# Kernel tuning notes

Hardware: AMD Instinct MI355X
Metric: run time of the kernel (lower is better)

## Reference

```python
import jax, jax.numpy as jnp
import numpy as np

KERNEL_MUL = 2.0
KERNEL_NUM = 5


def _index_matrix(b: int) -> jnp.ndarray:
    # non-linear JMMD index matrix (linear=False)
    im = np.zeros((2 * b, 2 * b), dtype=np.float32)
    off = 1.0 / float(b * (b - 1))
    eye = np.eye(b, dtype=bool)
    im[:b, :b][~eye] = off
    im[b:, b:][~eye] = off
    im[:b, b:] = -1.0 / float(b * b)
    im[b:, :b] = -1.0 / float(b * b)
    return jnp.asarray(im)


def _gaussian_kernel(source, target):
    total = jnp.concatenate([source, target], axis=0)  # [2b, d]
    n = total.shape[0]
    sq = jnp.sum(total * total, axis=1)  # [2b]
    # pairwise squared L2 via Gram matrix (same math as expand/diff/sum)
    l2 = sq[:, None] + sq[None, :] - 2.0 * (total @ total.T)
    l2 = jnp.maximum(l2, 0.0)
    # bandwidth computed on detached distances (torch uses .data)
    bw = jax.lax.stop_gradient(jnp.sum(l2)) / float(n * n - n)
    bw = bw / (KERNEL_MUL ** (KERNEL_NUM // 2))
    k = jnp.zeros_like(l2)
    for i in range(KERNEL_NUM):
        k = k + jnp.exp(-l2 / (bw * (KERNEL_MUL ** i)))
    return k


def setup_inputs() -> dict:
    key = jax.random.key(0)
    k1, k2, k3, k4 = jax.random.split(key, 4)
    b, d1, d2 = 2048, 4096, 2048
    return {
        "z1_s": jax.random.normal(k1, (b, d1), dtype=jnp.float32),
        "z1_t": jax.random.normal(k2, (b, d1), dtype=jnp.float32),
        "z2_s": jax.random.normal(k3, (b, d2), dtype=jnp.float32),
        "z2_t": jax.random.normal(k4, (b, d2), dtype=jnp.float32),
    }


def reference(z1_s, z1_t, z2_s, z2_t):
    b = z1_s.shape[0]
    index_matrix = _index_matrix(b)  # [2b, 2b]
    kernel_matrix = _gaussian_kernel(z1_s, z1_t) * _gaussian_kernel(z2_s, z2_t)
    loss = jnp.sum(kernel_matrix * index_matrix) + 2.0 / float(b - 1)
    return loss
```

## Files before the change

### kernel.cpp

```cpp
#include <hip/hip_runtime.h>
#include <cstdint>

#define NTOT 4096
#define BHALF 2048
#define D1 4096
#define D2 2048
#define TT 32
#define NTILES 528

typedef __attribute__((ext_vector_type(4))) float f32x4;
typedef __attribute__((ext_vector_type(4))) int i32x4;
typedef __attribute__((ext_vector_type(8))) int i32x8;

__device__ __forceinline__ void glds16(const uint8_t* g, uint8_t* l) {
    __builtin_amdgcn_global_load_lds(
        (const __attribute__((address_space(1))) void*)(uintptr_t)g,
        (__attribute__((address_space(3))) void*)(uint32_t)(uintptr_t)l,
        16, 0, 0);
}

__device__ __forceinline__ i32x4 ldsr(uint32_t addr) {
    i32x4 r;
    asm volatile("ds_read_b128 %0, %1" : "=v"(r) : "v"(addr));
    return r;
}

__device__ __forceinline__ float fp8dec(unsigned b) {
    unsigned e = (b >> 3) & 15u, m = b & 7u;
    float v = e ? __uint_as_float(((e + 120u) << 23) | (m << 20))
                : (float)m * 0.001953125f;
    return (b & 128u) ? -v : v;
}

__global__ void prep_kernel(const float* __restrict__ z1s, const float* __restrict__ z1t,
                            const float* __restrict__ z2s, const float* __restrict__ z2t,
                            float* __restrict__ sq1, float* __restrict__ sq2,
                            uint8_t* __restrict__ t1f8, uint8_t* __restrict__ t2f8,
                            float* __restrict__ s1, float* __restrict__ s2) {
    int bid = blockIdx.x;
    int tid = threadIdx.x;
    if (bid == 0) { for (int i = tid; i < 4096; i += 256) s1[i] = 0.f; }
    if (bid == 1) { for (int i = tid; i < 2048; i += 256) s2[i] = 0.f; }
    int which = bid >> 12;
    int row = bid & 4095;
    int d = which ? D2 : D1;
    const float* s_ = which ? z2s : z1s;
    const float* t_ = which ? z2t : z1t;
    const float* src = (row < BHALF) ? s_ + (size_t)row * d : t_ + (size_t)(row - BHALF) * d;
    uint8_t* dst = (which ? t2f8 : t1f8) + (size_t)row * d;
    float* sq = which ? sq2 : sq1;
    const float4* src4 = (const float4*)src;
    float a = 0.f;
    int n8 = d >> 3;
    for (int i = tid; i < n8; i += 256) {
        float4 v0 = src4[2 * i], v1 = src4[2 * i + 1];
        a += v0.x * v0.x + v0.y * v0.y + v0.z * v0.z + v0.w * v0.w;
        a += v1.x * v1.x + v1.y * v1.y + v1.z * v1.z + v1.w * v1.w;
        int w0 = __builtin_amdgcn_cvt_pk_fp8_f32(v0.x, v0.y, 0, 0);
        w0 = __builtin_amdgcn_cvt_pk_fp8_f32(v0.z, v0.w, w0, 1);
        int w1 = __builtin_amdgcn_cvt_pk_fp8_f32(v1.x, v1.y, 0, 0);
        w1 = __builtin_amdgcn_cvt_pk_fp8_f32(v1.z, v1.w, w1, 1);
        ((uint2*)dst)[i] = uint2{(unsigned)w0, (unsigned)w1};
    }
    for (int o = 32; o; o >>= 1) a += __shfl_down(a, o);
    __shared__ float sh[4];
    int lane = tid & 63, w = tid >> 6;
    if (lane == 0) sh[w] = a;
    __syncthreads();
    if (tid == 0) sq[row] = sh[0] + sh[1] + sh[2] + sh[3];
}

__global__ void colsum_fp8_kernel(const uint8_t* __restrict__ t1f8,
                                  const uint8_t* __restrict__ t2f8,
                                  float* __restrict__ s1, float* __restrict__ s2) {
    int bid = blockIdx.x;
    int which = bid >= 256;
    int local = which ? bid - 256 : bid;
    int d = which ? D2 : D1;
    int colchunks = d >> 10;
    int cb = local % colchunks, rb = local / colchunks;
    const uint8_t* base = which ? t2f8 : t1f8;
    float* s = which ? s2 : s1;
    int col = (cb << 10) + threadIdx.x * 4;
    int r0 = rb * 64;
    float a0 = 0.f, a1 = 0.f, a2 = 0.f, a3 = 0.f;
    const uint8_t* p = base + (size_t)r0 * d + col;
#pragma unroll 4
    for (int r = 0; r < 64; ++r) {
        uchar4 u = *(const uchar4*)(p + (size_t)r * d);
        a0 += fp8dec(u.x); a1 += fp8dec(u.y); a2 += fp8dec(u.z); a3 += fp8dec(u.w);
    }
    atomicAdd(&s[col], a0); atomicAdd(&s[col + 1], a1);
    atomicAdd(&s[col + 2], a2); atomicAdd(&s[col + 3], a3);
}

__global__ void finalize_kernel(const float* __restrict__ s1, const float* __restrict__ s2,
                                const float* __restrict__ sq1, const float* __restrict__ sq2,
                                float* __restrict__ acc, float* __restrict__ out) {
    int tid = threadIdx.x;
    float a1 = 0.f, a2 = 0.f, q1 = 0.f, q2 = 0.f;
    for (int i = tid; i < 4096; i += 256) { float v = s1[i]; a1 += v * v; q1 += sq1[i]; q2 += sq2[i]; }
    for (int i = tid; i < 2048; i += 256) { float v = s2[i]; a2 += v * v; }
    for (int o = 32; o; o >>= 1) {
        a1 += __shfl_down(a1, o); a2 += __shfl_down(a2, o);
        q1 += __shfl_down(q1, o); q2 += __shfl_down(q2, o);
    }
    __shared__ float sh[4][4];
    int lane = tid & 63, w = tid >> 6;
    if (lane == 0) { sh[0][w] = a1; sh[1][w] = a2; sh[2][w] = q1; sh[3][w] = q2; }
    __syncthreads();
    if (tid == 0) {
        double ss1 = (double)sh[0][0] + sh[0][1] + sh[0][2] + sh[0][3];
        double ss2 = (double)sh[1][0] + sh[1][1] + sh[1][2] + sh[1][3];
        double t1 = (double)sh[2][0] + sh[2][1] + sh[2][2] + sh[2][3];
        double t2 = (double)sh[3][0] + sh[3][1] + sh[3][2] + sh[3][3];
        double S1 = 2.0 * (double)NTOT * t1 - 2.0 * ss1;
        double S2 = 2.0 * (double)NTOT * t2 - 2.0 * ss2;
        const double L2E = 1.4426950408889634;
        double nn = (double)NTOT * (double)(NTOT - 1);
        acc[2] = (float)(nn * L2E / (4.0 * S1));
        acc[3] = (float)(nn * L2E / (4.0 * S2));
        out[0] = 2.0f / (float)(BHALF - 1);
    }
}

__device__ __forceinline__ void gemm_mx_pipe(const uint8_t* __restrict__ ga,
                                             const uint8_t* __restrict__ gb,
                                             int d,
                                             uint8_t* A0, uint8_t* B0,
                                             uint8_t* A1, uint8_t* B1,
                                             f32x4 (&acc)[4][4], int wv, int lane,
                                             int wm, int wn, int lm, int quad) {
    int nsteps = d >> 7;
    int rsub = lane >> 3;
    int ql = (lane & 7) ^ rsub;
    const uint8_t* pa = ga + (size_t)(wv * 32 + rsub) * d + ql * 16;
    const uint8_t* pb = gb + (size_t)(wv * 32 + rsub) * d + ql * 16;
    uint8_t* dA[2] = { A0 + wv * 4096, A1 + wv * 4096 };
    uint8_t* dB[2] = { B0 + wv * 4096, B1 + wv * 4096 };
    uint32_t baseA[2] = { (uint32_t)(uintptr_t)A0, (uint32_t)(uintptr_t)A1 };
    uint32_t baseB[2] = { (uint32_t)(uintptr_t)B0, (uint32_t)(uintptr_t)B1 };
    int s0 = ((2 * quad) ^ (lm & 7)) * 16;
    int s1 = ((2 * quad + 1) ^ (lm & 7)) * 16;
    uint32_t offA[4], offB[4];
#pragma unroll
    for (int i = 0; i < 4; ++i) {
        offA[i] = (uint32_t)((wm * 64 + i * 16 + lm) * 128);
        offB[i] = (uint32_t)((wn * 64 + i * 16 + lm) * 128);
    }
#pragma unroll
    for (int i = 0; i < 4; ++i) {
        glds16(pa + (size_t)i * 8 * d, dA[0] + i * 1024);
        glds16(pb + (size_t)i * 8 * d, dB[0] + i * 1024);
    }
    for (int k = 0; k < nsteps; ++k) {
        int cur = k & 1, nxt = cur ^ 1;
        size_t koff = (size_t)((k + 1 < nsteps) ? (k + 1) : 0) << 7;
#pragma unroll
        for (int i = 0; i < 4; ++i) {
            glds16(pa + koff + (size_t)i * 8 * d, dA[nxt] + i * 1024);
            glds16(pb + koff + (size_t)i * 8 * d, dB[nxt] + i * 1024);
        }
        asm volatile("s_waitcnt vmcnt(8)\n\ts_barrier" ::: "memory");
        i32x4 a00, a01, a10, a11, a20, a21, a30, a31;
        i32x4 b00, b01, b10, b11, b20, b21, b30, b31;
        a00 = ldsr(baseA[cur] + offA[0] + s0); a01 = ldsr(baseA[cur] + offA[0] + s1);
        a10 = ldsr(baseA[cur] + offA[1] + s0); a11 = ldsr(baseA[cur] + offA[1] + s1);
        a20 = ldsr(baseA[cur] + offA[2] + s0); a21 = ldsr(baseA[cur] + offA[2] + s1);
        a30 = ldsr(baseA[cur] + offA[3] + s0); a31 = ldsr(baseA[cur] + offA[3] + s1);
        b00 = ldsr(baseB[cur] + offB[0] + s0); b01 = ldsr(baseB[cur] + offB[0] + s1);
        b10 = ldsr(baseB[cur] + offB[1] + s0); b11 = ldsr(baseB[cur] + offB[1] + s1);
        b20 = ldsr(baseB[cur] + offB[2] + s0); b21 = ldsr(baseB[cur] + offB[2] + s1);
        b30 = ldsr(baseB[cur] + offB[3] + s0); b31 = ldsr(baseB[cur] + offB[3] + s1);
        asm volatile("s_waitcnt lgkmcnt(0)"
                     : "+v"(a00), "+v"(a01), "+v"(a10), "+v"(a11),
                       "+v"(a20), "+v"(a21), "+v"(a30), "+v"(a31),
                       "+v"(b00), "+v"(b01), "+v"(b10), "+v"(b11),
                       "+v"(b20), "+v"(b21), "+v"(b30), "+v"(b31));
        union F { i32x4 h[2]; i32x8 v; };
        F ua[4], ub[4];
        ua[0].h[0] = a00; ua[0].h[1] = a01; ua[1].h[0] = a10; ua[1].h[1] = a11;
        ua[2].h[0] = a20; ua[2].h[1] = a21; ua[3].h[0] = a30; ua[3].h[1] = a31;
        ub[0].h[0] = b00; ub[0].h[1] = b01; ub[1].h[0] = b10; ub[1].h[1] = b11;
        ub[2].h[0] = b20; ub[2].h[1] = b21; ub[3].h[0] = b30; ub[3].h[1] = b31;
#pragma unroll
        for (int ni = 0; ni < 4; ++ni)
#pragma unroll
            for (int mi = 0; mi < 4; ++mi)
                acc[mi][ni] = __builtin_amdgcn_mfma_scale_f32_16x16x128_f8f6f4(
                    ua[mi].v, ub[ni].v, acc[mi][ni], 0, 0, 0, 0x7F7F7F7F, 0, 0x7F7F7F7F);
        asm volatile("s_barrier" ::: "memory");
    }
}

__global__ __launch_bounds__(256, 2) void jmmd_fused(
    const uint8_t* __restrict__ t1f8, const uint8_t* __restrict__ t2f8,
    const float* __restrict__ sq1, const float* __restrict__ sq2,
    const float* __restrict__ cv, float* __restrict__ out) {
    __shared__ alignas(16) uint8_t smem[4][16384];
    __shared__ float sqi1[128], sqj1[128], sqi2[128], sqj2[128];
    __shared__ float red[4];
    int tid = threadIdx.x;
    int ti = 0, r = blockIdx.x;
    while (r >= TT - ti) { r -= TT - ti; ++ti; }
    int tj = ti + r;
    int i0 = ti * 128, j0 = tj * 128;
    if (tid < 128) {
        sqi1[tid] = sq1[i0 + tid]; sqj1[tid] = sq1[j0 + tid];
        sqi2[tid] = sq2[i0 + tid]; sqj2[tid] = sq2[j0 + tid];
    }
    int lane = tid & 63, wv = tid >> 6;
    int wm = wv >> 1, wn = wv & 1, lm = lane & 15, quad = lane >> 4;
    f32x4 acc1[4][4] = {};
    f32x4 acc2[4][4] = {};
    gemm_mx_pipe(t1f8 + (size_t)i0 * D1, t1f8 + (size_t)j0 * D1, D1,
                 smem[0], smem[1], smem[2], smem[3], acc1, wv, lane, wm, wn, lm, quad);
    asm volatile("s_waitcnt vmcnt(0)\n\ts_barrier" ::: "memory");
    gemm_mx_pipe(t2f8 + (size_t)i0 * D2, t2f8 + (size_t)j0 * D2, D2,
                 smem[0], smem[1], smem[2], smem[3], acc2, wv, lane, wm, wn, lm, quad);
    float c1 = cv[0], c2 = cv[1];
    float local = 0.f;
    bool diag = (ti == tj);
#pragma unroll
    for (int mi = 0; mi < 4; ++mi) {
        int rbase = wm * 64 + mi * 16 + quad * 4;
#pragma unroll
        for (int ni = 0; ni < 4; ++ni) {
            int col = wn * 64 + ni * 16 + lm;
            float sb1 = sqj1[col], sb2 = sqj2[col];
#pragma unroll
            for (int rr = 0; rr < 4; ++rr) {
                int row = rbase + rr;
                float l2a = fmaxf(sqi1[row] + sb1 - 2.f * acc1[mi][ni][rr], 0.f);
                float l2b = fmaxf(sqi2[row] + sb2 - 2.f * acc2[mi][ni][rr], 0.f);
                float t1 = __builtin_amdgcn_exp2f(-l2a * c1);
                float k1 = t1; float u1 = t1 * t1; k1 += u1; u1 *= u1; k1 += u1; u1 *= u1; k1 += u1; u1 *= u1; k1 += u1;
                float t2 = __builtin_amdgcn_exp2f(-l2b * c2);
                float k2 = t2; float u2 = t2 * t2; k2 += u2; u2 *= u2; k2 += u2; u2 *= u2; k2 += u2; u2 *= u2; k2 += u2;
                float v = k1 * k2;
                if (diag && (row == col)) v = 0.f;
                local += v;
            }
        }
    }
    for (int o = 32; o; o >>= 1) local += __shfl_down(local, o);
    if (lane == 0) red[wv] = local;
    __syncthreads();
    if (tid == 0) {
        bool same = (i0 < BHALF) == (j0 < BHALF);
        float w = same ? (1.0f / ((float)BHALF * (float)(BHALF - 1)))
                       : (-1.0f / ((float)BHALF * (float)BHALF));
        if (!diag) w *= 2.f;
        atomicAdd(out, (red[0] + red[1] + red[2] + red[3]) * w);
    }
}

extern "C" void kernel_launch(void* const* d_in, const int* in_sizes, int n_in,
                              void* d_out, int out_size, void* d_ws, size_t ws_size,
                              hipStream_t stream) {
    const float* z1s = (const float*)d_in[0];
    const float* z1t = (const float*)d_in[1];
    const float* z2s = (const float*)d_in[2];
    const float* z2t = (const float*)d_in[3];
    float* out = (float*)d_out;

    float* ws = (float*)d_ws;
    float* sq1 = ws;
    float* sq2 = ws + 4096;
    float* s1  = ws + 8192;
    float* s2  = ws + 12288;
    float* acc = ws + 14336;
    uint8_t* t1f8 = (uint8_t*)(ws + 14344);
    uint8_t* t2f8 = t1f8 + (size_t)NTOT * D1;

    prep_kernel<<<8192, 256, 0, stream>>>(z1s, z1t, z2s, z2t, sq1, sq2, t1f8, t2f8, s1, s2);
    colsum_fp8_kernel<<<384, 256, 0, stream>>>(t1f8, t2f8, s1, s2);
    finalize_kernel<<<1, 256, 0, stream>>>(s1, s2, sq1, sq2, acc, out);
    jmmd_fused<<<NTILES, 256, 0, stream>>>(t1f8, t2f8, sq1, sq2, acc + 2, out);
}
```

Measured before the change: 277.3 us.

## Interleave LDS reads with MFMA in GEMM loop, merge prep rows, widen colsum loads

The GEMM inner loop now issues LDS reads in staged groups and waits on partial lgkmcnt counts. This lets the first MFMAs start while later fragments are still loading, and it raises wave priority around the MFMA groups. The prep kernel now handles both feature sets per row in one block, which halves the number of blocks. The column-sum kernel uses 16-byte loads with 16 accumulators per thread and fewer blocks. Fewer colsum blocks (96) may underfill the GPU, and more accumulator registers could raise register pressure.

```diff
diff --git a/kernel.cpp b/kernel.cpp
--- a/kernel.cpp
+++ b/kernel.cpp
@@ -37,61 +37,92 @@
                             float* __restrict__ sq1, float* __restrict__ sq2,
                             uint8_t* __restrict__ t1f8, uint8_t* __restrict__ t2f8,
                             float* __restrict__ s1, float* __restrict__ s2) {
-    int bid = blockIdx.x;
+    int row = blockIdx.x;
     int tid = threadIdx.x;
-    if (bid == 0) { for (int i = tid; i < 4096; i += 256) s1[i] = 0.f; }
-    if (bid == 1) { for (int i = tid; i < 2048; i += 256) s2[i] = 0.f; }
-    int which = bid >> 12;
-    int row = bid & 4095;
-    int d = which ? D2 : D1;
-    const float* s_ = which ? z2s : z1s;
-    const float* t_ = which ? z2t : z1t;
-    const float* src = (row < BHALF) ? s_ + (size_t)row * d : t_ + (size_t)(row - BHALF) * d;
-    uint8_t* dst = (which ? t2f8 : t1f8) + (size_t)row * d;
-    float* sq = which ? sq2 : sq1;
-    const float4* src4 = (const float4*)src;
-    float a = 0.f;
-    int n8 = d >> 3;
-    for (int i = tid; i < n8; i += 256) {
-        float4 v0 = src4[2 * i], v1 = src4[2 * i + 1];
-        a += v0.x * v0.x + v0.y * v0.y + v0.z * v0.z + v0.w * v0.w;
-        a += v1.x * v1.x + v1.y * v1.y + v1.z * v1.z + v1.w * v1.w;
-        int w0 = __builtin_amdgcn_cvt_pk_fp8_f32(v0.x, v0.y, 0, 0);
-        w0 = __builtin_amdgcn_cvt_pk_fp8_f32(v0.z, v0.w, w0, 1);
-        int w1 = __builtin_amdgcn_cvt_pk_fp8_f32(v1.x, v1.y, 0, 0);
-        w1 = __builtin_amdgcn_cvt_pk_fp8_f32(v1.z, v1.w, w1, 1);
-        ((uint2*)dst)[i] = uint2{(unsigned)w0, (unsigned)w1};
-    }
-    for (int o = 32; o; o >>= 1) a += __shfl_down(a, o);
-    __shared__ float sh[4];
+    if (row == 0) { for (int i = tid; i < 4096; i += 256) s1[i] = 0.f; }
+    if (row == 1) { for (int i = tid; i < 2048; i += 256) s2[i] = 0.f; }
+    bool lower = row < BHALF;
+    const float* src1 = lower ? z1s + (size_t)row * D1 : z1t + (size_t)(row - BHALF) * D1;
+    const float* src2 = lower ? z2s + (size_t)row * D2 : z2t + (size_t)(row - BHALF) * D2;
+    uint8_t* dst1 = t1f8 + (size_t)row * D1;
+    uint8_t* dst2 = t2f8 + (size_t)row * D2;
+    float a1 = 0.f, a2 = 0.f;
+    {
+        const float4* s4 = (const float4*)src1;
+        for (int i = tid; i < (D1 >> 3); i += 256) {
+            float4 v0 = s4[2 * i], v1 = s4[2 * i + 1];
+            a1 += v0.x * v0.x + v0.y * v0.y + v0.z * v0.z + v0.w * v0.w;
+            a1 += v1.x * v1.x + v1.y * v1.y + v1.z * v1.z + v1.w * v1.w;
+            int w0 = __builtin_amdgcn_cvt_pk_fp8_f32(v0.x, v0.y, 0, 0);
+            w0 = __builtin_amdgcn_cvt_pk_fp8_f32(v0.z, v0.w, w0, 1);
+            int w1 = __builtin_amdgcn_cvt_pk_fp8_f32(v1.x, v1.y, 0, 0);
+            w1 = __builtin_amdgcn_cvt_pk_fp8_f32(v1.z, v1.w, w1, 1);
+            ((uint2*)dst1)[i] = uint2{(unsigned)w0, (unsigned)w1};
+        }
+    }
+    {
+        const float4* s4 = (const float4*)src2;
+        for (int i = tid; i < (D2 >> 3); i += 256) {
+            float4 v0 = s4[2 * i], v1 = s4[2 * i + 1];
+            a2 += v0.x * v0.x + v0.y * v0.y + v0.z * v0.z + v0.w * v0.w;
+            a2 += v1.x * v1.x + v1.y * v1.y + v1.z * v1.z + v1.w * v1.w;
+            int w0 = __builtin_amdgcn_cvt_pk_fp8_f32(v0.x, v0.y, 0, 0);
+            w0 = __builtin_amdgcn_cvt_pk_fp8_f32(v0.z, v0.w, w0, 1);
+            int w1 = __builtin_amdgcn_cvt_pk_fp8_f32(v1.x, v1.y, 0, 0);
+            w1 = __builtin_amdgcn_cvt_pk_fp8_f32(v1.z, v1.w, w1, 1);
+            ((uint2*)dst2)[i] = uint2{(unsigned)w0, (unsigned)w1};
+        }
+    }
+    for (int o = 32; o; o >>= 1) {
+        a1 += __shfl_down(a1, o);
+        a2 += __shfl_down(a2, o);
+    }
+    __shared__ float sh[2][4];
     int lane = tid & 63, w = tid >> 6;
-    if (lane == 0) sh[w] = a;
+    if (lane == 0) { sh[0][w] = a1; sh[1][w] = a2; }
     __syncthreads();
-    if (tid == 0) sq[row] = sh[0] + sh[1] + sh[2] + sh[3];
+    if (tid == 0) {
+        sq1[row] = sh[0][0] + sh[0][1] + sh[0][2] + sh[0][3];
+        sq2[row] = sh[1][0] + sh[1][1] + sh[1][2] + sh[1][3];
+    }
 }
 
 __global__ void colsum_fp8_kernel(const uint8_t* __restrict__ t1f8,
                                   const uint8_t* __restrict__ t2f8,
                                   float* __restrict__ s1, float* __restrict__ s2) {
     int bid = blockIdx.x;
-    int which = bid >= 256;
-    int local = which ? bid - 256 : bid;
-    int d = which ? D2 : D1;
-    int colchunks = d >> 10;
-    int cb = local % colchunks, rb = local / colchunks;
-    const uint8_t* base = which ? t2f8 : t1f8;
-    float* s = which ? s2 : s1;
-    int col = (cb << 10) + threadIdx.x * 4;
-    int r0 = rb * 64;
-    float a0 = 0.f, a1 = 0.f, a2 = 0.f, a3 = 0.f;
+    int tid = threadIdx.x;
+    const uint8_t* base;
+    float* s;
+    int d, stripe, col;
+    if (bid < 64) {
+        base = t1f8; s = s1; d = D1;
+        stripe = bid; col = tid * 16;
+    } else {
+        base = t2f8; s = s2; d = D2;
+        int lb = bid - 64;
+        stripe = lb * 2 + (tid >> 7);
+        col = (tid & 127) * 16;
+    }
+    int r0 = stripe * 64;
     const uint8_t* p = base + (size_t)r0 * d + col;
+    float a[16];
+#pragma unroll
+    for (int i = 0; i < 16; ++i) a[i] = 0.f;
 #pragma unroll 4
     for (int r = 0; r < 64; ++r) {
-        uchar4 u = *(const uchar4*)(p + (size_t)r * d);
-        a0 += fp8dec(u.x); a1 += fp8dec(u.y); a2 += fp8dec(u.z); a3 += fp8dec(u.w);
-    }
-    atomicAdd(&s[col], a0); atomicAdd(&s[col + 1], a1);
-    atomicAdd(&s[col + 2], a2); atomicAdd(&s[col + 3], a3);
+        uint4 u = *(const uint4*)(p + (size_t)r * d);
+        unsigned w0 = u.x, w1 = u.y, w2 = u.z, w3 = u.w;
+#pragma unroll
+        for (int k = 0; k < 4; ++k) {
+            a[0 + k]  += fp8dec((w0 >> (8 * k)) & 255u);
+            a[4 + k]  += fp8dec((w1 >> (8 * k)) & 255u);
+            a[8 + k]  += fp8dec((w2 >> (8 * k)) & 255u);
+            a[12 + k] += fp8dec((w3 >> (8 * k)) & 255u);
+        }
+    }
+#pragma unroll
+    for (int i = 0; i < 16; ++i) atomicAdd(&s[col + i], a[i]);
 }
 
 __global__ void finalize_kernel(const float* __restrict__ s1, const float* __restrict__ s2,
@@ -162,34 +193,54 @@
             glds16(pb + koff + (size_t)i * 8 * d, dB[nxt] + i * 1024);
         }
         asm volatile("s_waitcnt vmcnt(8)\n\ts_barrier" ::: "memory");
-        i32x4 a00, a01, a10, a11, a20, a21, a30, a31;
-        i32x4 b00, b01, b10, b11, b20, b21, b30, b31;
-        a00 = ldsr(baseA[cur] + offA[0] + s0); a01 = ldsr(baseA[cur] + offA[0] + s1);
-        a10 = ldsr(baseA[cur] + offA[1] + s0); a11 = ldsr(baseA[cur] + offA[1] + s1);
-        a20 = ldsr(baseA[cur] + offA[2] + s0); a21 = ldsr(baseA[cur] + offA[2] + s1);
-        a30 = ldsr(baseA[cur] + offA[3] + s0); a31 = ldsr(baseA[cur] + offA[3] + s1);
-        b00 = ldsr(baseB[cur] + offB[0] + s0); b01 = ldsr(baseB[cur] + offB[0] + s1);
-        b10 = ldsr(baseB[cur] + offB[1] + s0); b11 = ldsr(baseB[cur] + offB[1] + s1);
-        b20 = ldsr(baseB[cur] + offB[2] + s0); b21 = ldsr(baseB[cur] + offB[2] + s1);
-        b30 = ldsr(baseB[cur] + offB[3] + s0); b31 = ldsr(baseB[cur] + offB[3] + s1);
+        i32x4 b00 = ldsr(baseB[cur] + offB[0] + s0), b01 = ldsr(baseB[cur] + offB[0] + s1);
+        i32x4 b10 = ldsr(baseB[cur] + offB[1] + s0), b11 = ldsr(baseB[cur] + offB[1] + s1);
+        i32x4 a00 = ldsr(baseA[cur] + offA[0] + s0), a01 = ldsr(baseA[cur] + offA[0] + s1);
+        i32x4 a10 = ldsr(baseA[cur] + offA[1] + s0), a11 = ldsr(baseA[cur] + offA[1] + s1);
+        i32x4 b20 = ldsr(baseB[cur] + offB[2] + s0), b21 = ldsr(baseB[cur] + offB[2] + s1);
+        i32x4 b30 = ldsr(baseB[cur] + offB[3] + s0), b31 = ldsr(baseB[cur] + offB[3] + s1);
+        i32x4 a20 = ldsr(baseA[cur] + offA[2] + s0), a21 = ldsr(baseA[cur] + offA[2] + s1);
+        i32x4 a30 = ldsr(baseA[cur] + offA[3] + s0), a31 = ldsr(baseA[cur] + offA[3] + s1);
+        union F { i32x4 h[2]; i32x8 v; };
+        F ua0, ua1, ua2, ua3, ub0, ub1, ub2, ub3;
+        asm volatile("s_waitcnt lgkmcnt(8)"
+                     : "+v"(b00), "+v"(b01), "+v"(b10), "+v"(b11),
+                       "+v"(a00), "+v"(a01), "+v"(a10), "+v"(a11));
+        __builtin_amdgcn_sched_barrier(0);
+        ub0.h[0] = b00; ub0.h[1] = b01; ub1.h[0] = b10; ub1.h[1] = b11;
+        ua0.h[0] = a00; ua0.h[1] = a01; ua1.h[0] = a10; ua1.h[1] = a11;
+        __builtin_amdgcn_s_setprio(1);
+        acc[0][0] = __builtin_amdgcn_mfma_scale_f32_16x16x128_f8f6f4(ua0.v, ub0.v, acc[0][0], 0, 0, 0, 0x7F7F7F7F, 0, 0x7F7F7F7F);
+        acc[0][1] = __builtin_amdgcn_mfma_scale_f32_16x16x128_f8f6f4(ua0.v, ub1.v, acc[0][1], 0, 0, 0, 0x7F7F7F7F, 0, 0x7F7F7F7F);
+        acc[1][0] = __builtin_amdgcn_mfma_scale_f32_16x16x128_f8f6f4(ua1.v, ub0.v, acc[1][0], 0, 0, 0, 0x7F7F7F7F, 0, 0x7F7F7F7F);
+        acc[1][1] = __builtin_amdgcn_mfma_scale_f32_16x16x128_f8f6f4(ua1.v, ub1.v, acc[1][1], 0, 0, 0, 0x7F7F7F7F, 0, 0x7F7F7F7F);
+        __builtin_amdgcn_s_setprio(0);
+        asm volatile("s_waitcnt lgkmcnt(4)"
+                     : "+v"(b20), "+v"(b21), "+v"(b30), "+v"(b31));
+        __builtin_amdgcn_sched_barrier(0);
+        ub2.h[0] = b20; ub2.h[1] = b21; ub3.h[0] = b30; ub3.h[1] = b31;
+        __builtin_amdgcn_s_setprio(1);
+        acc[0][2] = __builtin_amdgcn_mfma_scale_f32_16x16x128_f8f6f4(ua0.v, ub2.v, acc[0][2], 0, 0, 0, 0x7F7F7F7F, 0, 0x7F7F7F7F);
+        acc[0][3] = __builtin_amdgcn_mfma_scale_f32_16x16x128_f8f6f4(ua0.v, ub3.v, acc[0][3], 0, 0, 0, 0x7F7F7F7F, 0, 0x7F7F7F7F);
+        acc[1][2] = __builtin_amdgcn_mfma_scale_f32_16x16x128_f8f6f4(ua1.v, ub2.v, acc[1][2], 0, 0, 0, 0x7F7F7F7F, 0, 0x7F7F7F7F);
+        acc[1][3] = __builtin_amdgcn_mfma_scale_f32_16x16x128_f8f6f4(ua1.v, ub3.v, acc[1][3], 0, 0, 0, 0x7F7F7F7F, 0, 0x7F7F7F7F);
+        __builtin_amdgcn_s_setprio(0);
         asm volatile("s_waitcnt lgkmcnt(0)"
-                     : "+v"(a00), "+v"(a01), "+v"(a10), "+v"(a11),
-                       "+v"(a20), "+v"(a21), "+v"(a30), "+v"(a31),
-                       "+v"(b00), "+v"(b01), "+v"(b10), "+v"(b11),
-                       "+v"(b20), "+v"(b21), "+v"(b30), "+v"(b31));
-        union F { i32x4 h[2]; i32x8 v; };
-        F ua[4], ub[4];
-        ua[0].h[0] = a00; ua[0].h[1] = a01; ua[1].h[0] = a10; ua[1].h[1] = a11;
-        ua[2].h[0] = a20; ua[2].h[1] = a21; ua[3].h[0] = a30; ua[3].h[1] = a31;
-        ub[0].h[0] = b00; ub[0].h[1] = b01; ub[1].h[0] = b10; ub[1].h[1] = b11;
-        ub[2].h[0] = b20; ub[2].h[1] = b21; ub[3].h[0] = b30; ub[3].h[1] = b31;
-#pragma unroll
-        for (int ni = 0; ni < 4; ++ni)
-#pragma unroll
-            for (int mi = 0; mi < 4; ++mi)
-                acc[mi][ni] = __builtin_amdgcn_mfma_scale_f32_16x16x128_f8f6f4(
-                    ua[mi].v, ub[ni].v, acc[mi][ni], 0, 0, 0, 0x7F7F7F7F, 0, 0x7F7F7F7F);
+                     : "+v"(a20), "+v"(a21), "+v"(a30), "+v"(a31));
+        __builtin_amdgcn_sched_barrier(0);
         asm volatile("s_barrier" ::: "memory");
+        __builtin_amdgcn_sched_barrier(0);
+        ua2.h[0] = a20; ua2.h[1] = a21; ua3.h[0] = a30; ua3.h[1] = a31;
+        __builtin_amdgcn_s_setprio(1);
+        acc[2][0] = __builtin_amdgcn_mfma_scale_f32_16x16x128_f8f6f4(ua2.v, ub0.v, acc[2][0], 0, 0, 0, 0x7F7F7F7F, 0, 0x7F7F7F7F);
+        acc[2][1] = __builtin_amdgcn_mfma_scale_f32_16x16x128_f8f6f4(ua2.v, ub1.v, acc[2][1], 0, 0, 0, 0x7F7F7F7F, 0, 0x7F7F7F7F);
+        acc[2][2] = __builtin_amdgcn_mfma_scale_f32_16x16x128_f8f6f4(ua2.v, ub2.v, acc[2][2], 0, 0, 0, 0x7F7F7F7F, 0, 0x7F7F7F7F);
+        acc[2][3] = __builtin_amdgcn_mfma_scale_f32_16x16x128_f8f6f4(ua2.v, ub3.v, acc[2][3], 0, 0, 0, 0x7F7F7F7F, 0, 0x7F7F7F7F);
+        acc[3][0] = __builtin_amdgcn_mfma_scale_f32_16x16x128_f8f6f4(ua3.v, ub0.v, acc[3][0], 0, 0, 0, 0x7F7F7F7F, 0, 0x7F7F7F7F);
+        acc[3][1] = __builtin_amdgcn_mfma_scale_f32_16x16x128_f8f6f4(ua3.v, ub1.v, acc[3][1], 0, 0, 0, 0x7F7F7F7F, 0, 0x7F7F7F7F);
+        acc[3][2] = __builtin_amdgcn_mfma_scale_f32_16x16x128_f8f6f4(ua3.v, ub2.v, acc[3][2], 0, 0, 0, 0x7F7F7F7F, 0, 0x7F7F7F7F);
+        acc[3][3] = __builtin_amdgcn_mfma_scale_f32_16x16x128_f8f6f4(ua3.v, ub3.v, acc[3][3], 0, 0, 0, 0x7F7F7F7F, 0, 0x7F7F7F7F);
+        __builtin_amdgcn_s_setprio(0);
     }
 }
 
@@ -273,8 +324,8 @@
     uint8_t* t1f8 = (uint8_t*)(ws + 14344);
     uint8_t* t2f8 = t1f8 + (size_t)NTOT * D1;
 
-    prep_kernel<<<8192, 256, 0, stream>>>(z1s, z1t, z2s, z2t, sq1, sq2, t1f8, t2f8, s1, s2);
-    colsum_fp8_kernel<<<384, 256, 0, stream>>>(t1f8, t2f8, s1, s2);
+    prep_kernel<<<4096, 256, 0, stream>>>(z1s, z1t, z2s, z2t, sq1, sq2, t1f8, t2f8, s1, s2);
+    colsum_fp8_kernel<<<96, 256, 0, stream>>>(t1f8, t2f8, s1, s2);
     finalize_kernel<<<1, 256, 0, stream>>>(s1, s2, sq1, sq2, acc, out);
     jmmd_fused<<<NTILES, 256, 0, stream>>>(t1f8, t2f8, sq1, sq2, acc + 2, out);
 }
```

After: 326.1 us. +17.6%, slower.
